# Kernel optimization log

Hardware: AMD Instinct MI355X
Metric: run time of the kernel (lower is better)

Reference implementation:

```python
import jax, jax.numpy as jnp
import numpy as np


def setup_inputs() -> dict:
    key = jax.random.key(0)
    ks = jax.random.split(key, 12)
    N, E, G = 100000, 1000000, 64
    D = 64            # node/edge/global feature dim
    IN = 4 * D        # concat: edge + receiver + sender + global = 256
    H, OUT = 128, 128 # latent_sizes, n_feat_out
    x = jax.random.normal(ks[0], (N, D), dtype=jnp.float32)
    e = jax.random.normal(ks[1], (E, D), dtype=jnp.float32)
    u = jax.random.normal(ks[2], (G, D), dtype=jnp.float32)
    edge_index = jax.random.randint(ks[3], (2, E), 0, N, dtype=jnp.int64)
    batch = jnp.sort(jax.random.randint(ks[4], (N,), 0, G, dtype=jnp.int64))
    s1 = 1.0 / np.sqrt(IN)
    s2 = 1.0 / np.sqrt(H)
    W1 = jax.random.uniform(ks[5], (IN, H), minval=-s1, maxval=s1, dtype=jnp.float32)
    b1 = jax.random.uniform(ks[6], (H,), minval=-s1, maxval=s1, dtype=jnp.float32)
    W2 = jax.random.uniform(ks[7], (H, OUT), minval=-s2, maxval=s2, dtype=jnp.float32)
    b2 = jax.random.uniform(ks[8], (OUT,), minval=-s2, maxval=s2, dtype=jnp.float32)
    ln_g = jnp.ones((OUT,), dtype=jnp.float32)
    ln_b = jnp.zeros((OUT,), dtype=jnp.float32)
    return {"x": x, "e": e, "u": u, "W1": W1, "b1": b1, "W2": W2, "b2": b2,
            "ln_g": ln_g, "ln_b": ln_b, "edge_index": edge_index, "batch": batch}


def _layernorm(h, g, b, eps=1e-5):
    mu = jnp.mean(h, axis=-1, keepdims=True)
    var = jnp.mean(jnp.square(h - mu), axis=-1, keepdims=True)
    return (h - mu) * jax.lax.rsqrt(var + eps) * g + b


def reference(x, e, u, W1, b1, W2, b2, ln_g, ln_b, edge_index, batch):
    row, col = edge_index[0], edge_index[1]
    sender = x[row]                    # [E, D]
    receiver = x[col]                  # [E, D]
    glob = u[batch[row]]               # globals scattered to edges [E, D]
    attrs = jnp.concatenate([e, receiver, sender, glob], axis=1)  # [E, 4D]
    h = jax.nn.relu(attrs @ W1 + b1)   # hidden layer
    h = jax.nn.relu(h @ W2 + b2)       # activate_final=True
    out = _layernorm(h, ln_g, ln_b)    # normalize=True
    return out
```

## Files before the change

kernel.cpp:

```cpp
#include <hip/hip_runtime.h>

typedef __bf16 bf16x8 __attribute__((ext_vector_type(8)));
typedef float  f32x4  __attribute__((ext_vector_type(4)));

struct alignas(8) U16x4 { unsigned short x, y, z, w; };

__device__ __forceinline__ unsigned short f2bf(float f) {
    union { float f; unsigned u; } v; v.f = f;
    unsigned u = v.u;
    return (unsigned short)((u + 0x7fffu + ((u >> 16) & 1u)) >> 16);
}

__global__ __launch_bounds__(256) void prep_weights(
    const float* __restrict__ W1, const float* __restrict__ W2,
    unsigned short* __restrict__ W1t, unsigned short* __restrict__ W2t)
{
    int tid = blockIdx.x * 256 + threadIdx.x;
    if (tid < 128 * 256) {
        int n = tid >> 8, k = tid & 255;
        W1t[tid] = f2bf(W1[k * 128 + n]);
    } else if (tid < 128 * 256 + 128 * 128) {
        int t = tid - 128 * 256;
        int n = t >> 7, k = t & 127;
        W2t[t] = f2bf(W2[k * 128 + n]);
    }
}

#define ETILE 64

__global__ __launch_bounds__(256) void edge_mlp(
    const float* __restrict__ x, const float* __restrict__ e, const float* __restrict__ u,
    const float* __restrict__ b1, const float* __restrict__ b2,
    const float* __restrict__ ln_g, const float* __restrict__ ln_b,
    const int* __restrict__ edge_index, const int* __restrict__ batch,
    const unsigned short* __restrict__ W1t, const unsigned short* __restrict__ W2t,
    float* __restrict__ out, int E)
{
    __shared__ __align__(16) unsigned short sA[ETILE * 256];
    __shared__ __align__(16) unsigned short sH[4][16 * 128];
    __shared__ int sRow[ETILE], sCol[ETILE], sG[ETILE];

    const int tid  = threadIdx.x;
    const int e0   = blockIdx.x * ETILE;
    const int wave = tid >> 6;
    const int lane = tid & 63;
    const int lrow = lane & 15;
    const int lk   = (lane >> 4) * 8;

    if (tid < ETILE) {
        int eid = e0 + tid;
        int eidc = eid < E ? eid : (E - 1);
        int r = edge_index[eidc];
        int c = edge_index[E + eidc];
        sRow[tid] = r; sCol[tid] = c; sG[tid] = batch[r];
    }
    __syncthreads();

    #pragma unroll
    for (int i = 0; i < 16; ++i) {
        int idx  = i * 256 + tid;
        int seg  = idx >> 10;
        int rem  = idx & 1023;
        int edge = rem >> 4;
        int p    = rem & 15;
        const float* src;
        if (seg == 0) {
            int ee = e0 + edge; if (ee >= E) ee = E - 1;
            src = e + (size_t)ee * 64 + p * 4;
        } else if (seg == 1) {
            src = x + (size_t)sCol[edge] * 64 + p * 4;
        } else if (seg == 2) {
            src = x + (size_t)sRow[edge] * 64 + p * 4;
        } else {
            src = u + (size_t)sG[edge] * 64 + p * 4;
        }
        float4 v = *(const float4*)src;
        U16x4 b; b.x = f2bf(v.x); b.y = f2bf(v.y); b.z = f2bf(v.z); b.w = f2bf(v.w);
        int bo = edge * 512 + seg * 128 + p * 8;
        bo ^= (edge & 7) << 4;
        *(U16x4*)((char*)sA + bo) = b;
    }
    __syncthreads();

    f32x4 acc[8];
    #pragma unroll
    for (int n = 0; n < 8; ++n) acc[n] = (f32x4){0.f, 0.f, 0.f, 0.f};

    const int m_base = wave * 16;
    #pragma unroll
    for (int kk = 0; kk < 8; ++kk) {
        int m  = m_base + lrow;
        int bo = m * 512 + (kk * 32 + lk) * 2;
        bo ^= (m & 7) << 4;
        bf16x8 a = *(const bf16x8*)((const char*)sA + bo);
        #pragma unroll
        for (int n = 0; n < 8; ++n) {
            bf16x8 b = *(const bf16x8*)(W1t + (n * 16 + lrow) * 256 + kk * 32 + lk);
            acc[n] = __builtin_amdgcn_mfma_f32_16x16x32_bf16(a, b, acc[n], 0, 0, 0);
        }
    }

    float bias1[8];
    #pragma unroll
    for (int n = 0; n < 8; ++n) bias1[n] = b1[n * 16 + lrow];

    unsigned short* hbuf = sH[wave];
    #pragma unroll
    for (int n = 0; n < 8; ++n) {
        #pragma unroll
        for (int r = 0; r < 4; ++r) {
            float v = acc[n][r] + bias1[n];
            v = v > 0.f ? v : 0.f;
            int row = (lane >> 4) * 4 + r;
            int col = n * 16 + lrow;
            int bo  = row * 256 + col * 2;
            bo ^= (row & 7) << 4;
            *(unsigned short*)((char*)hbuf + bo) = f2bf(v);
        }
    }
    __syncthreads();

    f32x4 acc2[8];
    #pragma unroll
    for (int n = 0; n < 8; ++n) acc2[n] = (f32x4){0.f, 0.f, 0.f, 0.f};

    #pragma unroll
    for (int kk = 0; kk < 4; ++kk) {
        int bo = lrow * 256 + (kk * 32 + lk) * 2;
        bo ^= (lrow & 7) << 4;
        bf16x8 a = *(const bf16x8*)((const char*)hbuf + bo);
        #pragma unroll
        for (int n = 0; n < 8; ++n) {
            bf16x8 b = *(const bf16x8*)(W2t + (n * 16 + lrow) * 128 + kk * 32 + lk);
            acc2[n] = __builtin_amdgcn_mfma_f32_16x16x32_bf16(a, b, acc2[n], 0, 0, 0);
        }
    }

    float bias2[8], g_[8], bb_[8];
    #pragma unroll
    for (int n = 0; n < 8; ++n) {
        bias2[n] = b2[n * 16 + lrow];
        g_[n]    = ln_g[n * 16 + lrow];
        bb_[n]   = ln_b[n * 16 + lrow];
    }

    float v[8][4];
    #pragma unroll
    for (int n = 0; n < 8; ++n)
        #pragma unroll
        for (int r = 0; r < 4; ++r) {
            float t = acc2[n][r] + bias2[n];
            v[n][r] = t > 0.f ? t : 0.f;
        }

    #pragma unroll
    for (int r = 0; r < 4; ++r) {
        float s = 0.f, s2 = 0.f;
        #pragma unroll
        for (int n = 0; n < 8; ++n) { s += v[n][r]; s2 += v[n][r] * v[n][r]; }
        #pragma unroll
        for (int m = 1; m < 16; m <<= 1) {
            s  += __shfl_xor(s,  m, 64);
            s2 += __shfl_xor(s2, m, 64);
        }
        float mu   = s * (1.f / 128.f);
        float var  = s2 * (1.f / 128.f) - mu * mu;
        float rstd = rsqrtf(var + 1e-5f);

        int edge = e0 + m_base + (lane >> 4) * 4 + r;
        if (edge < E) {
            float* orow = out + (size_t)edge * 128;
            #pragma unroll
            for (int n = 0; n < 8; ++n)
                orow[n * 16 + lrow] = (v[n][r] - mu) * rstd * g_[n] + bb_[n];
        }
    }
}

extern "C" void kernel_launch(void* const* d_in, const int* in_sizes, int n_in,
                              void* d_out, int out_size, void* d_ws, size_t ws_size,
                              hipStream_t stream) {
    const float* x    = (const float*)d_in[0];
    const float* e    = (const float*)d_in[1];
    const float* u    = (const float*)d_in[2];
    const float* W1   = (const float*)d_in[3];
    const float* b1   = (const float*)d_in[4];
    const float* W2   = (const float*)d_in[5];
    const float* b2   = (const float*)d_in[6];
    const float* ln_g = (const float*)d_in[7];
    const float* ln_b = (const float*)d_in[8];
    const int*   edge_index = (const int*)d_in[9];
    const int*   batch      = (const int*)d_in[10];

    const int E = in_sizes[9] / 2;

    unsigned short* W1t = (unsigned short*)d_ws;
    unsigned short* W2t = W1t + 128 * 256;

    prep_weights<<<192, 256, 0, stream>>>(W1, W2, W1t, W2t);

    int nblk = (E + ETILE - 1) / ETILE;
    edge_mlp<<<nblk, 256, 0, stream>>>(x, e, u, b1, b2, ln_g, ln_b,
                                       edge_index, batch, W1t, W2t,
                                       (float*)d_out, E);
}
```

Baseline: 1.308 ms.

## Load gathered operands directly into registers and precast node features to bf16

Drops the shared-memory staging of the concatenated input tile. Each wave now handles 32 edges and gathers its MFMA A-operands straight from global memory into registers, with no block-wide syncs. A precast pass converts x and u to bf16 in the workspace, which halves the bytes moved by the random row gathers. The cost is an extra kernel launch and workspace use. Edge indices are no longer clamped or bounds-checked, so this relies on E being a multiple of 32.

```diff
diff --git a/kernel.cpp b/kernel.cpp
--- a/kernel.cpp
+++ b/kernel.cpp
@@ -1,19 +1,19 @@
 #include <hip/hip_runtime.h>
 
+typedef __bf16 bf16_t;
 typedef __bf16 bf16x8 __attribute__((ext_vector_type(8)));
 typedef float  f32x4  __attribute__((ext_vector_type(4)));
-
-struct alignas(8) U16x4 { unsigned short x, y, z, w; };
-
-__device__ __forceinline__ unsigned short f2bf(float f) {
+typedef unsigned short u16;
+
+__device__ __forceinline__ u16 f2bf(float f) {
     union { float f; unsigned u; } v; v.f = f;
     unsigned u = v.u;
-    return (unsigned short)((u + 0x7fffu + ((u >> 16) & 1u)) >> 16);
+    return (u16)((u + 0x7fffu + ((u >> 16) & 1u)) >> 16);
 }
 
 __global__ __launch_bounds__(256) void prep_weights(
     const float* __restrict__ W1, const float* __restrict__ W2,
-    unsigned short* __restrict__ W1t, unsigned short* __restrict__ W2t)
+    u16* __restrict__ W1t, u16* __restrict__ W2t)
 {
     int tid = blockIdx.x * 256 + threadIdx.x;
     if (tid < 128 * 256) {
@@ -26,77 +26,102 @@
     }
 }
 
-#define ETILE 64
-
-__global__ __launch_bounds__(256) void edge_mlp(
+__global__ __launch_bounds__(256) void prep_cast(
+    const float* __restrict__ x, const float* __restrict__ u,
+    bf16_t* __restrict__ xb, bf16_t* __restrict__ ub, int nx, int nu)
+{
+    int total = (nx + nu) >> 2;
+    for (int i = blockIdx.x * 256 + threadIdx.x; i < total; i += gridDim.x * 256) {
+        int j = i << 2;
+        const float* src; bf16_t* dst;
+        if (j < nx) { src = x + j;        dst = xb + j; }
+        else        { src = u + (j - nx); dst = ub + (j - nx); }
+        float4 v = *(const float4*)src;
+        dst[0] = (__bf16)v.x; dst[1] = (__bf16)v.y;
+        dst[2] = (__bf16)v.z; dst[3] = (__bf16)v.w;
+    }
+}
+
+__device__ __forceinline__ bf16x8 cvt8(const float* __restrict__ p) {
+    float4 a = *(const float4*)p;
+    float4 b = *(const float4*)(p + 4);
+    bf16x8 r;
+    r[0] = (__bf16)a.x; r[1] = (__bf16)a.y; r[2] = (__bf16)a.z; r[3] = (__bf16)a.w;
+    r[4] = (__bf16)b.x; r[5] = (__bf16)b.y; r[6] = (__bf16)b.z; r[7] = (__bf16)b.w;
+    return r;
+}
+
+template<bool PRECAST>
+__global__ __launch_bounds__(256, 4) void edge_mlp(
     const float* __restrict__ x, const float* __restrict__ e, const float* __restrict__ u,
+    const bf16_t* __restrict__ xb, const bf16_t* __restrict__ ub,
     const float* __restrict__ b1, const float* __restrict__ b2,
     const float* __restrict__ ln_g, const float* __restrict__ ln_b,
     const int* __restrict__ edge_index, const int* __restrict__ batch,
-    const unsigned short* __restrict__ W1t, const unsigned short* __restrict__ W2t,
+    const bf16_t* __restrict__ W1t, const bf16_t* __restrict__ W2t,
     float* __restrict__ out, int E)
 {
-    __shared__ __align__(16) unsigned short sA[ETILE * 256];
-    __shared__ __align__(16) unsigned short sH[4][16 * 128];
-    __shared__ int sRow[ETILE], sCol[ETILE], sG[ETILE];
-
-    const int tid  = threadIdx.x;
-    const int e0   = blockIdx.x * ETILE;
-    const int wave = tid >> 6;
-    const int lane = tid & 63;
+    __shared__ __align__(16) u16 sH[4][32 * 128];
+
+    const int wave = threadIdx.x >> 6;
+    const int lane = threadIdx.x & 63;
     const int lrow = lane & 15;
-    const int lk   = (lane >> 4) * 8;
-
-    if (tid < ETILE) {
-        int eid = e0 + tid;
-        int eidc = eid < E ? eid : (E - 1);
-        int r = edge_index[eidc];
-        int c = edge_index[E + eidc];
-        sRow[tid] = r; sCol[tid] = c; sG[tid] = batch[r];
-    }
-    __syncthreads();
-
-    #pragma unroll
-    for (int i = 0; i < 16; ++i) {
-        int idx  = i * 256 + tid;
-        int seg  = idx >> 10;
-        int rem  = idx & 1023;
-        int edge = rem >> 4;
-        int p    = rem & 15;
-        const float* src;
-        if (seg == 0) {
-            int ee = e0 + edge; if (ee >= E) ee = E - 1;
-            src = e + (size_t)ee * 64 + p * 4;
-        } else if (seg == 1) {
-            src = x + (size_t)sCol[edge] * 64 + p * 4;
-        } else if (seg == 2) {
-            src = x + (size_t)sRow[edge] * 64 + p * 4;
+    const int kg   = lane >> 4;
+    const int lk   = kg * 8;
+
+    const long tb = (long)(blockIdx.x * 4 + wave) * 32;
+    if (tb >= E) return;
+
+    const int eid0 = (int)tb + lrow;
+    const int eid1 = eid0 + 16;
+    const int r0 = edge_index[eid0],     r1 = edge_index[eid1];
+    const int c0 = edge_index[E + eid0], c1 = edge_index[E + eid1];
+    const int g0 = batch[r0],            g1 = batch[r1];
+
+    const float*  ep0 = e + (size_t)eid0 * 64;
+    const float*  ep1 = e + (size_t)eid1 * 64;
+
+    f32x4 acc[2][8] = {};
+
+    const bf16_t* w1b = W1t + lrow * 256 + lk;
+
+    #pragma unroll
+    for (int kk = 0; kk < 8; ++kk) {
+        const int off = (kk & 1) * 32 + lk;
+        bf16x8 a0, a1;
+        if (kk < 2) {
+            a0 = cvt8(ep0 + off);
+            a1 = cvt8(ep1 + off);
+        } else if (kk < 4) {
+            if (PRECAST) {
+                a0 = *(const bf16x8*)(xb + (size_t)c0 * 64 + off);
+                a1 = *(const bf16x8*)(xb + (size_t)c1 * 64 + off);
+            } else {
+                a0 = cvt8(x + (size_t)c0 * 64 + off);
+                a1 = cvt8(x + (size_t)c1 * 64 + off);
+            }
+        } else if (kk < 6) {
+            if (PRECAST) {
+                a0 = *(const bf16x8*)(xb + (size_t)r0 * 64 + off);
+                a1 = *(const bf16x8*)(xb + (size_t)r1 * 64 + off);
+            } else {
+                a0 = cvt8(x + (size_t)r0 * 64 + off);
+                a1 = cvt8(x + (size_t)r1 * 64 + off);
+            }
         } else {
-            src = u + (size_t)sG[edge] * 64 + p * 4;
-        }
-        float4 v = *(const float4*)src;
-        U16x4 b; b.x = f2bf(v.x); b.y = f2bf(v.y); b.z = f2bf(v.z); b.w = f2bf(v.w);
-        int bo = edge * 512 + seg * 128 + p * 8;
-        bo ^= (edge & 7) << 4;
-        *(U16x4*)((char*)sA + bo) = b;
-    }
-    __syncthreads();
-
-    f32x4 acc[8];
-    #pragma unroll
-    for (int n = 0; n < 8; ++n) acc[n] = (f32x4){0.f, 0.f, 0.f, 0.f};
-
-    const int m_base = wave * 16;
-    #pragma unroll
-    for (int kk = 0; kk < 8; ++kk) {
-        int m  = m_base + lrow;
-        int bo = m * 512 + (kk * 32 + lk) * 2;
-        bo ^= (m & 7) << 4;
-        bf16x8 a = *(const bf16x8*)((const char*)sA + bo);
+            if (PRECAST) {
+                a0 = *(const bf16x8*)(ub + (size_t)g0 * 64 + off);
+                a1 = *(const bf16x8*)(ub + (size_t)g1 * 64 + off);
+            } else {
+                a0 = cvt8(u + (size_t)g0 * 64 + off);
+                a1 = cvt8(u + (size_t)g1 * 64 + off);
+            }
+        }
         #pragma unroll
         for (int n = 0; n < 8; ++n) {
-            bf16x8 b = *(const bf16x8*)(W1t + (n * 16 + lrow) * 256 + kk * 32 + lk);
-            acc[n] = __builtin_amdgcn_mfma_f32_16x16x32_bf16(a, b, acc[n], 0, 0, 0);
+            bf16x8 b = *(const bf16x8*)(w1b + n * 16 * 256 + kk * 32);
+            acc[0][n] = __builtin_amdgcn_mfma_f32_16x16x32_bf16(a0, b, acc[0][n], 0, 0, 0);
+            acc[1][n] = __builtin_amdgcn_mfma_f32_16x16x32_bf16(a1, b, acc[1][n], 0, 0, 0);
         }
     }
 
@@ -104,77 +129,93 @@
     #pragma unroll
     for (int n = 0; n < 8; ++n) bias1[n] = b1[n * 16 + lrow];
 
-    unsigned short* hbuf = sH[wave];
-    #pragma unroll
-    for (int n = 0; n < 8; ++n) {
-        #pragma unroll
-        for (int r = 0; r < 4; ++r) {
-            float v = acc[n][r] + bias1[n];
-            v = v > 0.f ? v : 0.f;
-            int row = (lane >> 4) * 4 + r;
-            int col = n * 16 + lrow;
-            int bo  = row * 256 + col * 2;
+    u16* hb = sH[wave];
+    #pragma unroll
+    for (int m = 0; m < 2; ++m)
+        #pragma unroll
+        for (int n = 0; n < 8; ++n)
+            #pragma unroll
+            for (int r = 0; r < 4; ++r) {
+                float v = acc[m][n][r] + bias1[n];
+                v = v > 0.f ? v : 0.f;
+                int row = m * 16 + kg * 4 + r;
+                int bo  = row * 256 + (n * 16 + lrow) * 2;
+                bo ^= (row & 7) << 4;
+                *(u16*)((char*)hb + bo) = __builtin_bit_cast(u16, (__bf16)v);
+            }
+
+    asm volatile("s_waitcnt lgkmcnt(0)" ::: "memory");
+    __builtin_amdgcn_sched_barrier(0);
+
+    f32x4 acc2[2][8] = {};
+    const bf16_t* w2b = W2t + lrow * 128 + lk;
+
+    #pragma unroll
+    for (int kk = 0; kk < 4; ++kk) {
+        bf16x8 a0, a1;
+        {
+            int row = lrow;
+            int bo  = row * 256 + (kk * 32 + lk) * 2;
             bo ^= (row & 7) << 4;
-            *(unsigned short*)((char*)hbuf + bo) = f2bf(v);
-        }
-    }
-    __syncthreads();
-
-    f32x4 acc2[8];
-    #pragma unroll
-    for (int n = 0; n < 8; ++n) acc2[n] = (f32x4){0.f, 0.f, 0.f, 0.f};
-
-    #pragma unroll
-    for (int kk = 0; kk < 4; ++kk) {
-        int bo = lrow * 256 + (kk * 32 + lk) * 2;
-        bo ^= (lrow & 7) << 4;
-        bf16x8 a = *(const bf16x8*)((const char*)hbuf + bo);
+            a0 = *(const bf16x8*)((const char*)hb + bo);
+        }
+        {
+            int row = 16 + lrow;
+            int bo  = row * 256 + (kk * 32 + lk) * 2;
+            bo ^= (row & 7) << 4;
+            a1 = *(const bf16x8*)((const char*)hb + bo);
+        }
         #pragma unroll
         for (int n = 0; n < 8; ++n) {
-            bf16x8 b = *(const bf16x8*)(W2t + (n * 16 + lrow) * 128 + kk * 32 + lk);
-            acc2[n] = __builtin_amdgcn_mfma_f32_16x16x32_bf16(a, b, acc2[n], 0, 0, 0);
-        }
-    }
-
-    float bias2[8], g_[8], bb_[8];
+            bf16x8 b = *(const bf16x8*)(w2b + n * 16 * 128 + kk * 32);
+            acc2[0][n] = __builtin_amdgcn_mfma_f32_16x16x32_bf16(a0, b, acc2[0][n], 0, 0, 0);
+            acc2[1][n] = __builtin_amdgcn_mfma_f32_16x16x32_bf16(a1, b, acc2[1][n], 0, 0, 0);
+        }
+    }
+
+    float bias2[8], gg[8], bb[8];
     #pragma unroll
     for (int n = 0; n < 8; ++n) {
         bias2[n] = b2[n * 16 + lrow];
-        g_[n]    = ln_g[n * 16 + lrow];
-        bb_[n]   = ln_b[n * 16 + lrow];
-    }
-
-    float v[8][4];
-    #pragma unroll
-    for (int n = 0; n < 8; ++n)
+        gg[n]    = ln_g[n * 16 + lrow];
+        bb[n]    = ln_b[n * 16 + lrow];
+    }
+
+    #pragma unroll
+    for (int m = 0; m < 2; ++m)
+        #pragma unroll
+        for (int n = 0; n < 8; ++n)
+            #pragma unroll
+            for (int r = 0; r < 4; ++r) {
+                float t = acc2[m][n][r] + bias2[n];
+                acc2[m][n][r] = t > 0.f ? t : 0.f;
+            }
+
+    #pragma unroll
+    for (int m = 0; m < 2; ++m)
         #pragma unroll
         for (int r = 0; r < 4; ++r) {
-            float t = acc2[n][r] + bias2[n];
-            v[n][r] = t > 0.f ? t : 0.f;
-        }
-
-    #pragma unroll
-    for (int r = 0; r < 4; ++r) {
-        float s = 0.f, s2 = 0.f;
-        #pragma unroll
-        for (int n = 0; n < 8; ++n) { s += v[n][r]; s2 += v[n][r] * v[n][r]; }
-        #pragma unroll
-        for (int m = 1; m < 16; m <<= 1) {
-            s  += __shfl_xor(s,  m, 64);
-            s2 += __shfl_xor(s2, m, 64);
-        }
-        float mu   = s * (1.f / 128.f);
-        float var  = s2 * (1.f / 128.f) - mu * mu;
-        float rstd = rsqrtf(var + 1e-5f);
-
-        int edge = e0 + m_base + (lane >> 4) * 4 + r;
-        if (edge < E) {
+            float s = 0.f, s2 = 0.f;
+            #pragma unroll
+            for (int n = 0; n < 8; ++n) {
+                float v = acc2[m][n][r];
+                s += v; s2 += v * v;
+            }
+            #pragma unroll
+            for (int msk = 1; msk < 16; msk <<= 1) {
+                s  += __shfl_xor(s,  msk, 64);
+                s2 += __shfl_xor(s2, msk, 64);
+            }
+            float mu   = s * (1.f / 128.f);
+            float var  = s2 * (1.f / 128.f) - mu * mu;
+            float rstd = rsqrtf(var + 1e-5f);
+
+            long edge = tb + m * 16 + kg * 4 + r;
             float* orow = out + (size_t)edge * 128;
             #pragma unroll
             for (int n = 0; n < 8; ++n)
-                orow[n * 16 + lrow] = (v[n][r] - mu) * rstd * g_[n] + bb_[n];
-        }
-    }
+                orow[n * 16 + lrow] = (acc2[m][n][r] - mu) * rstd * gg[n] + bb[n];
+        }
 }
 
 extern "C" void kernel_launch(void* const* d_in, const int* in_sizes, int n_in,
@@ -192,15 +233,33 @@
     const int*   edge_index = (const int*)d_in[9];
     const int*   batch      = (const int*)d_in[10];
 
-    const int E = in_sizes[9] / 2;
-
-    unsigned short* W1t = (unsigned short*)d_ws;
-    unsigned short* W2t = W1t + 128 * 256;
+    const int E  = in_sizes[9] / 2;
+    const int nx = in_sizes[0];
+    const int nu = in_sizes[2];
+
+    u16* W1t = (u16*)d_ws;
+    u16* W2t = W1t + 128 * 256;
+    bf16_t* xbp = (bf16_t*)(W2t + 128 * 128);
+    bf16_t* ubp = xbp + nx;
+
+    size_t needed = 98304 + (size_t)(nx + nu) * 2;
+    bool precast = ws_size >= needed;
 
     prep_weights<<<192, 256, 0, stream>>>(W1, W2, W1t, W2t);
 
-    int nblk = (E + ETILE - 1) / ETILE;
-    edge_mlp<<<nblk, 256, 0, stream>>>(x, e, u, b1, b2, ln_g, ln_b,
-                                       edge_index, batch, W1t, W2t,
-                                       (float*)d_out, E);
-}
+    int nblk = (E + 127) / 128;
+    if (precast) {
+        int cgrid = ((nx + nu) / 4 + 255) / 256;
+        if (cgrid > 2048) cgrid = 2048;
+        prep_cast<<<cgrid, 256, 0, stream>>>(x, u, xbp, ubp, nx, nu);
+        edge_mlp<true><<<nblk, 256, 0, stream>>>(x, e, u, xbp, ubp, b1, b2, ln_g, ln_b,
+                                                 edge_index, batch,
+                                                 (const bf16_t*)W1t, (const bf16_t*)W2t,
+                                                 (float*)d_out, E);
+    } else {
+        edge_mlp<false><<<nblk, 256, 0, stream>>>(x, e, u, nullptr, nullptr, b1, b2, ln_g, ln_b,
+                                                  edge_index, batch,
+                                                  (const bf16_t*)W1t, (const bf16_t*)W2t,
+                                                  (float*)d_out, E);
+    }
+}
```

After: 1.077 ms. 1.21x faster.
